# Performance work log

Hardware: AMD Instinct MI355X
Metric: run time of the kernel (lower is better)

## Reference

```python
import jax, jax.numpy as jnp
import numpy as np


def setup_inputs() -> dict:
    key = jax.random.key(0)
    kx, kw = jax.random.split(key)
    A_MAX = 16  # activations in [0, 2**A_bits - 1] = [0, 15]
    W_MAX = 15  # torch.randint(0, 2**W_bits - 1) -> [0, 14]
    x = jax.random.randint(kx, (32, 256, 56, 56), 0, A_MAX, dtype=jnp.int32)
    weight = jax.random.randint(kw, (256, 256, 3, 3), 0, W_MAX, dtype=jnp.int32)
    return {"x": x, "weight": weight}


def reference(x, weight):
    # Low-bit quantized conv2d: direct_conv2d(x.int(), w.int(), stride=1) with the
    # module's crop for (k=3, padding=1) is equivalent to a conv with padding=1.
    # Max accumulator value = 15*14*9*256 < 2**24, so fp32 accumulation is exact.
    xf = x.astype(jnp.float32)
    wf = weight.astype(jnp.float32)
    y = jax.lax.conv_general_dilated(
        xf, wf,
        window_strides=(1, 1),
        padding=((1, 1), (1, 1)),
        dimension_numbers=("NCHW", "OIHW", "NCHW"),
    )
    return y.astype(jnp.int32)  # [32, 256, 56, 56]
```

## Files before the change

kernel.cpp:

```cpp
#include <hip/hip_runtime.h>

typedef int v4i  __attribute__((ext_vector_type(4)));
typedef int v16i __attribute__((ext_vector_type(16)));

#define N_IMG   32
#define C_IN    256
#define HWDIM   56
#define HW2     3136
#define OUT_TOT 25690112
#define OUT_NSTR 802816

#define PXB     272
#define PPI     3364
#define XP_IMG  915008
#define WP_CB2STR 73728
#define WP_BYTES  589824ull

#define S_TILE  256
#define TILES_PER_IMG 13
#define WIN_PX  384
#define WIN_B   104448
#define XP_SLACK WIN_B

__global__ void dc_x_to_nhwc(const int* __restrict__ x, unsigned int* __restrict__ x8,
                             int n0) {
    __shared__ unsigned int lds[64 * 65];
    const int t = threadIdx.x;
    const int w = t & 63, q = t >> 6;
    const int nl = blockIdx.x / HWDIM, h = blockIdx.x % HWDIM;

    if (w < HWDIM) {
        const int* xb = x + (size_t)(n0 + nl) * OUT_NSTR + h * HWDIM + w;
        #pragma unroll
        for (int it = 0; it < 16; ++it) {
            const int cg4 = q * 16 + it;
            const int ci0 = cg4 * 4;
            unsigned v  =  ((unsigned)xb[(ci0 + 0) * HW2] & 0xff);
            v |= ((unsigned)xb[(ci0 + 1) * HW2] & 0xff) << 8;
            v |= ((unsigned)xb[(ci0 + 2) * HW2] & 0xff) << 16;
            v |= ((unsigned)xb[(ci0 + 3) * HW2] & 0xff) << 24;
            lds[w * 65 + cg4] = v;
        }
    }
    __syncthreads();
    unsigned int* ob = x8 + (size_t)nl * (PPI * (PXB / 4)) + ((h + 1) * 58 + 1) * (PXB / 4);
    #pragma unroll
    for (int it = 0; it < 14; ++it) {
        const int f = it * 256 + t;
        const int w2 = f >> 6, cg = f & 63;
        if (w2 < HWDIM) ob[w2 * (PXB / 4) + cg] = lds[w2 * 65 + cg];
    }
}

__global__ void dc_halo(unsigned int* __restrict__ x8) {
    const int nl = blockIdx.x;
    const int t = threadIdx.x;
    if (t < 228) {
        int h, w;
        if (t < 58)       { h = 0;        w = t; }
        else if (t < 116) { h = 57;       w = t - 58; }
        else if (t < 172) { h = t - 115;  w = 0; }
        else              { h = t - 171;  w = 57; }
        unsigned int* p = x8 + ((size_t)nl * PPI + h * 58 + w) * (PXB / 4);
        #pragma unroll
        for (int i = 0; i < PXB / 4; ++i) p[i] = 0;
    }
}

__global__ void dc_pack_w(const int* __restrict__ wt, unsigned int* __restrict__ wp) {
    const int tid = blockIdx.x * 256 + threadIdx.x;
    const int jq = tid & 3;
    const int l  = (tid >> 2) & 63;
    const int kb = (tid >> 8) & 7;
    const int r  = tid >> 11;
    const int t  = r % 9;
    const int cb2 = r / 9;
    const int co  = cb2 * 32 + (l & 31);
    const int ci0 = kb * 32 + (l >> 5) * 16 + jq * 4;
    const int kh = t / 3, kw = t - kh * 3;
    unsigned v = 0;
    #pragma unroll
    for (int k = 0; k < 4; ++k) {
        unsigned b = (unsigned)wt[((co * C_IN + ci0 + k) * 3 + kh) * 3 + kw];
        v |= (b & 0xff) << (8 * k);
    }
    wp[tid] = v;
}

__device__ __forceinline__ void gll16(const char* g, char* l) {
    __builtin_amdgcn_global_load_lds(
        (const __attribute__((address_space(1))) unsigned int*)g,
        (__attribute__((address_space(3))) unsigned int*)l, 16, 0, 0);
}

__global__ __launch_bounds__(512, 2) void dc_mfma(const char* __restrict__ x8,
                                                  const char* __restrict__ wp,
                                                  int* __restrict__ out, int nwg) {
    extern __shared__ __align__(16) char xs[];

    const int bid = blockIdx.x;
    const int q = nwg >> 3, r = nwg & 7;
    const int xcd = bid & 7, bidx = bid >> 3;
    const int wgid = (xcd < r ? xcd * (q + 1) : r * (q + 1) + (xcd - r) * q) + bidx;

    const int nl = wgid / TILES_PER_IMG, st = wgid - nl * TILES_PER_IMG;

    const int tid = threadIdx.x;
    const int l = tid & 63, wid = tid >> 6;
    const int lane31 = l & 31, hi = l >> 5;
    const int cow = wid & 3, sgw = wid >> 2;

    const int hw0 = st * S_TILE;
    const int p0 = (hw0 / HWDIM + 1) * 58 + (hw0 % HWDIM) + 1 - 59;
    const char* gsrc = x8 + (size_t)nl * XP_IMG + (size_t)p0 * PXB;

    #pragma unroll
    for (int c = 0; c < 13; ++c) {
        const int off = (c * 512 + tid) * 16;
        if (off < WIN_B) gll16(gsrc + off, xs + off);
    }

    int breg[4], outb[4];
    bool val[4];
    #pragma unroll
    for (int ni = 0; ni < 4; ++ni) {
        int hw = hw0 + sgw * 128 + ni * 32 + lane31;
        val[ni] = (hw < HW2);
        if (!val[ni]) hw = HW2 - 1;
        const int p = (hw / HWDIM + 1) * 58 + (hw % HWDIM) + 1;
        breg[ni] = (p - p0) * PXB + hi * 16 - 16048;
        outb[ni] = nl * OUT_NSTR + hw;
    }

    const char* wb0 = wp + (cow * 2) * WP_CB2STR + l * 16;
    const char* wb1 = wb0 + WP_CB2STR;

    const int xoffp[9] = {
        16048 - 59 * PXB, 16048 - 58 * PXB, 16048 - 57 * PXB,
        16048 - 1 * PXB,  16048,            16048 + 1 * PXB,
        16048 + 57 * PXB, 16048 + 58 * PXB, 16048 + 59 * PXB
    };

    __syncthreads();

    v16i acc[2][4] = {};
    v4i wa[4][2];
    v4i xb[2][4];

    wa[0][0] = *(const v4i*)(wb0);
    wa[0][1] = *(const v4i*)(wb1);
    wa[1][0] = *(const v4i*)(wb0 + 1024);
    wa[1][1] = *(const v4i*)(wb1 + 1024);
    wa[2][0] = *(const v4i*)(wb0 + 2048);
    wa[2][1] = *(const v4i*)(wb1 + 2048);
    #pragma unroll
    for (int ni = 0; ni < 4; ++ni)
        xb[0][ni] = *(const v4i*)(xs + breg[ni] + xoffp[0]);

    #pragma unroll
    for (int j = 0; j < 72; ++j) {
        const int jc = j & 3;
        const int pc = j & 1;
        if (j + 3 < 72) {
            const int jn = (j + 3) & 3;
            wa[jn][0] = *(const v4i*)(wb0 + (j + 3) * 1024);
            wa[jn][1] = *(const v4i*)(wb1 + (j + 3) * 1024);
        }
        if (j + 1 < 72) {
            const int t1 = (j + 1) >> 3, kb1 = (j + 1) & 7;
            const int xo = xoffp[t1] + kb1 * 32;
            #pragma unroll
            for (int ni = 0; ni < 4; ++ni)
                xb[pc ^ 1][ni] = *(const v4i*)(xs + breg[ni] + xo);
        }
        __builtin_amdgcn_s_setprio(1);
        #pragma unroll
        for (int mi = 0; mi < 2; ++mi) {
            #pragma unroll
            for (int ni = 0; ni < 4; ++ni) {
                acc[mi][ni] = __builtin_amdgcn_mfma_i32_32x32x32_i8(
                    wa[jc][mi], xb[pc][ni], acc[mi][ni], 0, 0, 0);
            }
        }
        __builtin_amdgcn_s_setprio(0);
    }

    #pragma unroll
    for (int mi = 0; mi < 2; ++mi) {
        #pragma unroll
        for (int ni = 0; ni < 4; ++ni) {
            if (!val[ni]) continue;
            const v16i c = acc[mi][ni];
            int* ob = out + outb[ni] + (cow * 64 + mi * 32 + 4 * hi) * HW2;
            #pragma unroll
            for (int rr = 0; rr < 16; ++rr) {
                __builtin_nontemporal_store(c[rr], ob + ((rr & 3) + 8 * (rr >> 2)) * HW2);
            }
        }
    }
}

__global__ void dc_naive(const int* __restrict__ x, const int* __restrict__ wt,
                         int* __restrict__ out) {
    const int idx = blockIdx.x * 256 + threadIdx.x;
    if (idx >= OUT_TOT) return;
    const int w = idx % HWDIM;
    const int h = (idx / HWDIM) % HWDIM;
    const int co = (idx / HW2) & 255;
    const int n = idx / OUT_NSTR;
    const int* xn = x + n * OUT_NSTR;
    const int* wo = wt + co * (C_IN * 9);
    int acc = 0;
    for (int ci = 0; ci < C_IN; ++ci) {
        const int* xc = xn + ci * HW2;
        const int* wc = wo + ci * 9;
        #pragma unroll
        for (int kh = 0; kh < 3; ++kh) {
            const int hh = h + kh - 1;
            if ((unsigned)hh >= HWDIM) continue;
            #pragma unroll
            for (int kw = 0; kw < 3; ++kw) {
                const int ww = w + kw - 1;
                if ((unsigned)ww >= HWDIM) continue;
                acc += xc[hh * HWDIM + ww] * wc[kh * 3 + kw];
            }
        }
    }
    out[idx] = acc;
}

extern "C" void kernel_launch(void* const* d_in, const int* in_sizes, int n_in,
                              void* d_out, int out_size, void* d_ws, size_t ws_size,
                              hipStream_t stream) {
    const int* x  = (const int*)d_in[0];
    const int* wt = (const int*)d_in[1];
    int* out = (int*)d_out;

    int chunk = 0;
    const int cand[4] = {32, 16, 8, 4};
    for (int i = 0; i < 4; ++i) {
        if ((size_t)cand[i] * XP_IMG + XP_SLACK + WP_BYTES <= ws_size) { chunk = cand[i]; break; }
    }

    if (chunk > 0) {
        char* x8 = (char*)d_ws;
        const size_t x8_bytes = (size_t)chunk * XP_IMG + XP_SLACK;
        unsigned int* wp = (unsigned int*)(x8 + x8_bytes);
        hipLaunchKernelGGL(dc_halo, dim3(chunk), dim3(256), 0, stream, (unsigned int*)x8);
        hipLaunchKernelGGL(dc_pack_w, dim3(576), dim3(256), 0, stream, wt, wp);
        for (int n0 = 0; n0 < N_IMG; n0 += chunk) {
            hipLaunchKernelGGL(dc_x_to_nhwc, dim3(chunk * HWDIM), dim3(256), 0, stream,
                               x, (unsigned int*)x8, n0);
            const int nwg = chunk * TILES_PER_IMG;
            hipLaunchKernelGGL(dc_mfma, dim3(nwg), dim3(512), WIN_B, stream,
                               (const char*)x8, (const char*)wp,
                               out + (size_t)n0 * OUT_NSTR, nwg);
        }
        return;
    }

    hipLaunchKernelGGL(dc_naive, dim3((OUT_TOT + 255) / 256), dim3(256), 0, stream,
                       x, wt, out);
}
```

Before: 95.99 us.

## Stage weight tiles in LDS with double-buffered async global-to-LDS loads

Weight fragments were read by every wave straight from global memory with a register prefetch ring. Now the workgroup cooperatively copies each weight phase into a double-buffered LDS region using global_load_lds, and waves read their fragments from LDS. The aim is to remove duplicate global weight traffic across the two spatial wave groups and shorten load latency. The cost is a workgroup barrier in each of 36 phases, a larger LDS allocation, and loss of the x-operand register prefetch, so MFMA issue now waits on LDS reads.

```diff
diff --git a/kernel.cpp b/kernel.cpp
--- a/kernel.cpp
+++ b/kernel.cpp
@@ -18,9 +18,10 @@
 
 #define S_TILE  256
 #define TILES_PER_IMG 13
-#define WIN_PX  384
 #define WIN_B   104448
 #define XP_SLACK WIN_B
+#define WPHB    16384
+#define LDSB    (WIN_B + 2*WPHB)
 
 __global__ void dc_x_to_nhwc(const int* __restrict__ x, unsigned int* __restrict__ x8,
                              int n0) {
@@ -97,6 +98,7 @@
                                                   const char* __restrict__ wp,
                                                   int* __restrict__ out, int nwg) {
     extern __shared__ __align__(16) char xs[];
+    char* wbuf = xs + WIN_B;
 
     const int bid = blockIdx.x;
     const int q = nwg >> 3, r = nwg & 7;
@@ -108,7 +110,7 @@
     const int tid = threadIdx.x;
     const int l = tid & 63, wid = tid >> 6;
     const int lane31 = l & 31, hi = l >> 5;
-    const int cow = wid & 3, sgw = wid >> 2;
+    const int cg = wid & 3, sg = wid >> 2;
 
     const int hw0 = st * S_TILE;
     const int p0 = (hw0 / HWDIM + 1) * 58 + (hw0 % HWDIM) + 1 - 59;
@@ -120,11 +122,20 @@
         if (off < WIN_B) gll16(gsrc + off, xs + off);
     }
 
+    const int idx0 = tid, idx1 = 512 + tid;
+    const char* wsrc0 = wp + (idx0 >> 7) * WP_CB2STR + ((idx0 >> 6) & 1) * 1024 + (idx0 & 63) * 16;
+    const char* wsrc1 = wp + (idx1 >> 7) * WP_CB2STR + ((idx1 >> 6) & 1) * 1024 + (idx1 & 63) * 16;
+    char* wdst0 = wbuf + idx0 * 16;
+    char* wdst1 = wbuf + idx1 * 16;
+
+    gll16(wsrc0, wdst0);
+    gll16(wsrc1, wdst1);
+
     int breg[4], outb[4];
     bool val[4];
     #pragma unroll
     for (int ni = 0; ni < 4; ++ni) {
-        int hw = hw0 + sgw * 128 + ni * 32 + lane31;
+        int hw = hw0 + sg * 128 + ni * 32 + lane31;
         val[ni] = (hw < HW2);
         if (!val[ni]) hw = HW2 - 1;
         const int p = (hw / HWDIM + 1) * 58 + (hw % HWDIM) + 1;
@@ -132,9 +143,6 @@
         outb[ni] = nl * OUT_NSTR + hw;
     }
 
-    const char* wb0 = wp + (cow * 2) * WP_CB2STR + l * 16;
-    const char* wb1 = wb0 + WP_CB2STR;
-
     const int xoffp[9] = {
         16048 - 59 * PXB, 16048 - 58 * PXB, 16048 - 57 * PXB,
         16048 - 1 * PXB,  16048,            16048 + 1 * PXB,
@@ -144,45 +152,41 @@
     __syncthreads();
 
     v16i acc[2][4] = {};
-    v4i wa[4][2];
-    v4i xb[2][4];
-
-    wa[0][0] = *(const v4i*)(wb0);
-    wa[0][1] = *(const v4i*)(wb1);
-    wa[1][0] = *(const v4i*)(wb0 + 1024);
-    wa[1][1] = *(const v4i*)(wb1 + 1024);
-    wa[2][0] = *(const v4i*)(wb0 + 2048);
-    wa[2][1] = *(const v4i*)(wb1 + 2048);
-    #pragma unroll
-    for (int ni = 0; ni < 4; ++ni)
-        xb[0][ni] = *(const v4i*)(xs + breg[ni] + xoffp[0]);
-
-    #pragma unroll
-    for (int j = 0; j < 72; ++j) {
-        const int jc = j & 3;
-        const int pc = j & 1;
-        if (j + 3 < 72) {
-            const int jn = (j + 3) & 3;
-            wa[jn][0] = *(const v4i*)(wb0 + (j + 3) * 1024);
-            wa[jn][1] = *(const v4i*)(wb1 + (j + 3) * 1024);
-        }
-        if (j + 1 < 72) {
-            const int t1 = (j + 1) >> 3, kb1 = (j + 1) & 7;
-            const int xo = xoffp[t1] + kb1 * 32;
+
+    #pragma unroll
+    for (int p = 0; p < 36; ++p) {
+        const int t = p >> 2, kp = p & 3;
+        if (p < 35) {
+            const int pn = p + 1;
+            const int wso = (pn >> 2) * 8192 + (pn & 3) * 2048;
+            const int wdo = (pn & 1) * WPHB;
+            gll16(wsrc0 + wso, wdst0 + wdo);
+            gll16(wsrc1 + wso, wdst1 + wdo);
+        }
+        const char* wb = wbuf + (p & 1) * WPHB;
+        #pragma unroll
+        for (int kbl = 0; kbl < 2; ++kbl) {
+            const int kb = kp * 2 + kbl;
+            const int xo = xoffp[t] + kb * 32;
+            v4i xf[4], wf[2];
             #pragma unroll
             for (int ni = 0; ni < 4; ++ni)
-                xb[pc ^ 1][ni] = *(const v4i*)(xs + breg[ni] + xo);
-        }
-        __builtin_amdgcn_s_setprio(1);
-        #pragma unroll
-        for (int mi = 0; mi < 2; ++mi) {
-            #pragma unroll
-            for (int ni = 0; ni < 4; ++ni) {
-                acc[mi][ni] = __builtin_amdgcn_mfma_i32_32x32x32_i8(
-                    wa[jc][mi], xb[pc][ni], acc[mi][ni], 0, 0, 0);
+                xf[ni] = *(const v4i*)(xs + breg[ni] + xo);
+            #pragma unroll
+            for (int mi = 0; mi < 2; ++mi)
+                wf[mi] = *(const v4i*)(wb + ((2 * cg + mi) * 2 + kbl) * 1024 + l * 16);
+            __builtin_amdgcn_s_setprio(1);
+            #pragma unroll
+            for (int mi = 0; mi < 2; ++mi) {
+                #pragma unroll
+                for (int ni = 0; ni < 4; ++ni) {
+                    acc[mi][ni] = __builtin_amdgcn_mfma_i32_32x32x32_i8(
+                        wf[mi], xf[ni], acc[mi][ni], 0, 0, 0);
+                }
             }
-        }
-        __builtin_amdgcn_s_setprio(0);
+            __builtin_amdgcn_s_setprio(0);
+        }
+        __syncthreads();
     }
 
     #pragma unroll
@@ -191,7 +195,7 @@
         for (int ni = 0; ni < 4; ++ni) {
             if (!val[ni]) continue;
             const v16i c = acc[mi][ni];
-            int* ob = out + outb[ni] + (cow * 64 + mi * 32 + 4 * hi) * HW2;
+            int* ob = out + outb[ni] + (cg * 64 + mi * 32 + 4 * hi) * HW2;
             #pragma unroll
             for (int rr = 0; rr < 16; ++rr) {
                 __builtin_nontemporal_store(c[rr], ob + ((rr & 3) + 8 * (rr >> 2)) * HW2);
@@ -252,7 +256,7 @@
             hipLaunchKernelGGL(dc_x_to_nhwc, dim3(chunk * HWDIM), dim3(256), 0, stream,
                                x, (unsigned int*)x8, n0);
             const int nwg = chunk * TILES_PER_IMG;
-            hipLaunchKernelGGL(dc_mfma, dim3(nwg), dim3(512), WIN_B, stream,
+            hipLaunchKernelGGL(dc_mfma, dim3(nwg), dim3(512), LDSB, stream,
                                (const char*)x8, (const char*)wp,
                                out + (size_t)n0 * OUT_NSTR, nwg);
         }
```

New measurement: 105.7 us. +10.1%, slower.

## Shrink conv output tile to 64 pixels with 4-wave workgroups

Applied to the files above, without the earlier changes.

The spatial tile per workgroup drops from 256 to 64 output pixels, giving 49 tiles per image with no partial tile, and workgroups shrink from 8 waves to 4. Each wave now covers 64 output channels by 64 pixels, so it issues 4 MFMAs per step instead of 8, and the LDS halo window shrinks to about 50KB so three workgroups can share a CU. The aim is to remove tail waste and raise occupancy and wave count. The cost is more weight reloads per pixel, a larger share of the tile spent on halo rows, and fewer MFMAs per LDS load.

```diff
diff --git a/kernel.cpp b/kernel.cpp
--- a/kernel.cpp
+++ b/kernel.cpp
@@ -13,14 +13,13 @@
 #define PXB     272
 #define PPI     3364
 #define XP_IMG  915008
+#define XP_SLACK 4096
 #define WP_CB2STR 73728
 #define WP_BYTES  589824ull
 
-#define S_TILE  256
-#define TILES_PER_IMG 13
-#define WIN_PX  384
-#define WIN_B   104448
-#define XP_SLACK WIN_B
+#define S_TILE  64
+#define TILES_PER_IMG 49
+#define WIN_B   50048
 
 __global__ void dc_x_to_nhwc(const int* __restrict__ x, unsigned int* __restrict__ x8,
                              int n0) {
@@ -93,7 +92,7 @@
         (__attribute__((address_space(3))) unsigned int*)l, 16, 0, 0);
 }
 
-__global__ __launch_bounds__(512, 2) void dc_mfma(const char* __restrict__ x8,
+__global__ __launch_bounds__(256, 3) void dc_mfma(const char* __restrict__ x8,
                                                   const char* __restrict__ wp,
                                                   int* __restrict__ out, int nwg) {
     extern __shared__ __align__(16) char xs[];
@@ -108,31 +107,29 @@
     const int tid = threadIdx.x;
     const int l = tid & 63, wid = tid >> 6;
     const int lane31 = l & 31, hi = l >> 5;
-    const int cow = wid & 3, sgw = wid >> 2;
 
     const int hw0 = st * S_TILE;
-    const int p0 = (hw0 / HWDIM + 1) * 58 + (hw0 % HWDIM) + 1 - 59;
+    const int h0 = hw0 / HWDIM, w0 = hw0 - h0 * HWDIM;
+    const int p0 = h0 * 58 + w0;
     const char* gsrc = x8 + (size_t)nl * XP_IMG + (size_t)p0 * PXB;
 
     #pragma unroll
     for (int c = 0; c < 13; ++c) {
-        const int off = (c * 512 + tid) * 16;
+        const int off = (c * 256 + tid) * 16;
         if (off < WIN_B) gll16(gsrc + off, xs + off);
     }
 
-    int breg[4], outb[4];
-    bool val[4];
-    #pragma unroll
-    for (int ni = 0; ni < 4; ++ni) {
-        int hw = hw0 + sgw * 128 + ni * 32 + lane31;
-        val[ni] = (hw < HW2);
-        if (!val[ni]) hw = HW2 - 1;
-        const int p = (hw / HWDIM + 1) * 58 + (hw % HWDIM) + 1;
+    int breg[2], outb[2];
+    #pragma unroll
+    for (int ni = 0; ni < 2; ++ni) {
+        const int hw = hw0 + ni * 32 + lane31;
+        const int h = hw / HWDIM, w = hw - h * HWDIM;
+        const int p = (h + 1) * 58 + (w + 1);
         breg[ni] = (p - p0) * PXB + hi * 16 - 16048;
         outb[ni] = nl * OUT_NSTR + hw;
     }
 
-    const char* wb0 = wp + (cow * 2) * WP_CB2STR + l * 16;
+    const char* wb0 = wp + (wid * 2) * WP_CB2STR + l * 16;
     const char* wb1 = wb0 + WP_CB2STR;
 
     const int xoffp[9] = {
@@ -143,9 +140,9 @@
 
     __syncthreads();
 
-    v16i acc[2][4] = {};
+    v16i acc[2][2] = {};
     v4i wa[4][2];
-    v4i xb[2][4];
+    v4i xb[2][2];
 
     wa[0][0] = *(const v4i*)(wb0);
     wa[0][1] = *(const v4i*)(wb1);
@@ -153,9 +150,8 @@
     wa[1][1] = *(const v4i*)(wb1 + 1024);
     wa[2][0] = *(const v4i*)(wb0 + 2048);
     wa[2][1] = *(const v4i*)(wb1 + 2048);
-    #pragma unroll
-    for (int ni = 0; ni < 4; ++ni)
-        xb[0][ni] = *(const v4i*)(xs + breg[ni] + xoffp[0]);
+    xb[0][0] = *(const v4i*)(xs + breg[0] + xoffp[0]);
+    xb[0][1] = *(const v4i*)(xs + breg[1] + xoffp[0]);
 
     #pragma unroll
     for (int j = 0; j < 72; ++j) {
@@ -169,29 +165,23 @@
         if (j + 1 < 72) {
             const int t1 = (j + 1) >> 3, kb1 = (j + 1) & 7;
             const int xo = xoffp[t1] + kb1 * 32;
-            #pragma unroll
-            for (int ni = 0; ni < 4; ++ni)
-                xb[pc ^ 1][ni] = *(const v4i*)(xs + breg[ni] + xo);
+            xb[pc ^ 1][0] = *(const v4i*)(xs + breg[0] + xo);
+            xb[pc ^ 1][1] = *(const v4i*)(xs + breg[1] + xo);
         }
         __builtin_amdgcn_s_setprio(1);
-        #pragma unroll
-        for (int mi = 0; mi < 2; ++mi) {
-            #pragma unroll
-            for (int ni = 0; ni < 4; ++ni) {
-                acc[mi][ni] = __builtin_amdgcn_mfma_i32_32x32x32_i8(
-                    wa[jc][mi], xb[pc][ni], acc[mi][ni], 0, 0, 0);
-            }
-        }
+        acc[0][0] = __builtin_amdgcn_mfma_i32_32x32x32_i8(wa[jc][0], xb[pc][0], acc[0][0], 0, 0, 0);
+        acc[0][1] = __builtin_amdgcn_mfma_i32_32x32x32_i8(wa[jc][0], xb[pc][1], acc[0][1], 0, 0, 0);
+        acc[1][0] = __builtin_amdgcn_mfma_i32_32x32x32_i8(wa[jc][1], xb[pc][0], acc[1][0], 0, 0, 0);
+        acc[1][1] = __builtin_amdgcn_mfma_i32_32x32x32_i8(wa[jc][1], xb[pc][1], acc[1][1], 0, 0, 0);
         __builtin_amdgcn_s_setprio(0);
     }
 
     #pragma unroll
     for (int mi = 0; mi < 2; ++mi) {
         #pragma unroll
-        for (int ni = 0; ni < 4; ++ni) {
-            if (!val[ni]) continue;
+        for (int ni = 0; ni < 2; ++ni) {
             const v16i c = acc[mi][ni];
-            int* ob = out + outb[ni] + (cow * 64 + mi * 32 + 4 * hi) * HW2;
+            int* ob = out + outb[ni] + (wid * 64 + mi * 32 + 4 * hi) * HW2;
             #pragma unroll
             for (int rr = 0; rr < 16; ++rr) {
                 __builtin_nontemporal_store(c[rr], ob + ((rr & 3) + 8 * (rr >> 2)) * HW2);
@@ -252,7 +242,7 @@
             hipLaunchKernelGGL(dc_x_to_nhwc, dim3(chunk * HWDIM), dim3(256), 0, stream,
                                x, (unsigned int*)x8, n0);
             const int nwg = chunk * TILES_PER_IMG;
-            hipLaunchKernelGGL(dc_mfma, dim3(nwg), dim3(512), WIN_B, stream,
+            hipLaunchKernelGGL(dc_mfma, dim3(nwg), dim3(256), WIN_B, stream,
                                (const char*)x8, (const char*)wp,
                                out + (size_t)n0 * OUT_NSTR, nwg);
         }
```

Result: faster. 92.98 us (-3.1%).
